# Optimization experiments

Hardware: AMD Instinct MI355X
Metric: run time of the kernel (lower is better)

Reference implementation:

```python
import jax, jax.numpy as jnp
import numpy as np

B, T, D, H = 4, 2048, 1024, 16
DH = D // H


def setup_inputs() -> dict:
    key = jax.random.key(0)
    ks = jax.random.split(key, 5)
    x = jax.random.normal(ks[0], (B, T, D), dtype=jnp.float32)
    W_qkv = jax.random.normal(ks[1], (D, 3 * D), dtype=jnp.float32) * 0.02
    b_qkv = jax.random.normal(ks[2], (3 * D,), dtype=jnp.float32) * 0.02
    W_o = jax.random.normal(ks[3], (D, D), dtype=jnp.float32) * 0.02
    b_o = jax.random.normal(ks[4], (D,), dtype=jnp.float32) * 0.02
    return {"x": x, "W_qkv": W_qkv, "b_qkv": b_qkv, "W_o": W_o, "b_o": b_o}


def reference(x, W_qkv, b_qkv, W_o, b_o):
    b, t, d = x.shape
    qkv = x @ W_qkv + b_qkv                      # [b, t, 3*d]
    # 'b t (k h dh) -> k b h t dh'
    qkv = qkv.reshape(b, t, 3, H, DH).transpose(2, 0, 3, 1, 4)
    q, k, v = qkv[0], qkv[1], qkv[2]             # each [b, h, t, dh]
    scores = jnp.einsum('bhqd,bhkd->bhqk', q, k) / jnp.sqrt(jnp.float32(DH))
    causal_mask = jnp.triu(jnp.ones((t, t), dtype=bool), k=1)  # True above diag
    scores = jnp.where(causal_mask, -jnp.inf, scores)
    attn = jax.nn.softmax(scores, axis=-1)       # [b, h, t, t]
    o = jnp.einsum('bhqk,bhkd->bqhd', attn, v).reshape(b, t, d)
    return o @ W_o + b_o
```

## Files before the change

kernel.cpp:

```cpp
#include <hip/hip_runtime.h>
#include <hip/hip_bf16.h>

typedef __attribute__((ext_vector_type(8))) short bh8;
typedef __attribute__((ext_vector_type(4))) float f32x4;

#define GBL(p) (const __attribute__((address_space(1))) void*)(p)
#define LDSP(p) (__attribute__((address_space(3))) void*)(p)

__device__ __forceinline__ ushort f2bf(float f){
  union { float f; unsigned u; } v; v.f = f;
  unsigned u = v.u;
  return (ushort)((u + 0x7fffu + ((u >> 16) & 1u)) >> 16);
}

__global__ __launch_bounds__(256) void cast_x_kernel(const float4* __restrict__ in,
                                                     ushort* __restrict__ out){
  int i = blockIdx.x * 256 + threadIdx.x;
  float4 v = in[i];
  ushort4 o;
  o.x = f2bf(v.x); o.y = f2bf(v.y); o.z = f2bf(v.z); o.w = f2bf(v.w);
  *(ushort4*)&out[(size_t)i * 4] = o;
}

__global__ __launch_bounds__(256) void transpose_cast_kernel(const float* __restrict__ in,
                                                             ushort* __restrict__ out,
                                                             int R, int C){
  __shared__ float tile[32][33];
  int bx = blockIdx.x * 32;
  int by = blockIdx.y * 32;
  int tx = threadIdx.x, ty = threadIdx.y;
  #pragma unroll
  for (int i = 0; i < 32; i += 8)
    tile[ty + i][tx] = in[(size_t)(by + ty + i) * C + bx + tx];
  __syncthreads();
  #pragma unroll
  for (int i = 0; i < 32; i += 8)
    out[(size_t)(bx + ty + i) * R + by + tx] = f2bf(tile[tx][ty + i]);
}

__global__ __launch_bounds__(256) void gemm_qkv_kernel(
    const ushort* __restrict__ A,
    const ushort* __restrict__ Bt,
    const float* __restrict__ bias,
    ushort* __restrict__ Qd, ushort* __restrict__ Kd, ushort* __restrict__ Vt)
{
  constexpr int K = 1024;
  __shared__ ushort sA[8192];
  __shared__ ushort sB[8192];
  const int tid = threadIdx.x;
  const int lane = tid & 63, wave = tid >> 6;
  const int quad = lane >> 4, l16 = lane & 15;
  const int wm = (wave >> 1) * 64, wn = (wave & 1) * 64;
  const size_t aBase = (size_t)blockIdx.x * 128 * K;
  const size_t bBase = (size_t)blockIdx.y * 128 * K;
  f32x4 acc[4][4] = {};
  for (int k0 = 0; k0 < K; k0 += 64){
    #pragma unroll
    for (int c = 0; c < 4; c++){
      int u = c * 256 + tid;
      int ks = u >> 9, row = (u >> 2) & 127, q = u & 3;
      __builtin_amdgcn_global_load_lds(GBL(A + aBase + (size_t)row * K + k0 + ks * 32 + q * 8),
                                       LDSP(&sA[u * 8]), 16, 0, 0);
      __builtin_amdgcn_global_load_lds(GBL(Bt + bBase + (size_t)row * K + k0 + ks * 32 + q * 8),
                                       LDSP(&sB[u * 8]), 16, 0, 0);
    }
    __syncthreads();
    #pragma unroll
    for (int ks = 0; ks < 2; ks++){
      bh8 af[4], bf[4];
      #pragma unroll
      for (int i = 0; i < 4; i++) af[i] = *(const bh8*)&sA[ks * 4096 + (wm + i * 16 + l16) * 32 + quad * 8];
      #pragma unroll
      for (int j = 0; j < 4; j++) bf[j] = *(const bh8*)&sB[ks * 4096 + (wn + j * 16 + l16) * 32 + quad * 8];
      #pragma unroll
      for (int i = 0; i < 4; i++)
        #pragma unroll
        for (int j = 0; j < 4; j++)
          acc[i][j] = __builtin_amdgcn_mfma_f32_16x16x32_bf16(af[i], bf[j], acc[i][j], 0, 0, 0);
    }
    __syncthreads();
  }
  const int whichBlk = (blockIdx.y * 128) >> 10;
  #pragma unroll
  for (int i = 0; i < 4; i++){
    int mg = blockIdx.x * 128 + wm + i * 16 + quad * 4;
    int bb = mg >> 11, t0 = mg & 2047;
    #pragma unroll
    for (int j = 0; j < 4; j++){
      int ng = blockIdx.y * 128 + wn + j * 16 + l16;
      float bv = bias[ng];
      int h = (ng >> 6) & 15;
      int dh = ng & 63;
      if (whichBlk == 2){
        ushort4 o;
        o.x = f2bf(acc[i][j][0] + bv);
        o.y = f2bf(acc[i][j][1] + bv);
        o.z = f2bf(acc[i][j][2] + bv);
        o.w = f2bf(acc[i][j][3] + bv);
        *(ushort4*)&Vt[((size_t)((bb * 16 + h) * 64 + dh)) * 2048 + t0] = o;
      } else {
        ushort* dst = (whichBlk == 0) ? Qd : Kd;
        float sc = (whichBlk == 0) ? 0.125f : 1.0f;
        #pragma unroll
        for (int r = 0; r < 4; r++)
          dst[((size_t)((bb * 16 + h) * 2048 + t0 + r) << 6) + dh] = f2bf((acc[i][j][r] + bv) * sc);
      }
    }
  }
}

__global__ __launch_bounds__(256, 2) void flash_attn_kernel(
    const ushort* __restrict__ Qd, const ushort* __restrict__ Kd,
    const ushort* __restrict__ Vt, ushort* __restrict__ Od)
{
  __shared__ ushort sK[2][4096];
  __shared__ ushort sV[2][4096];
  __shared__ ushort sP[4][2][1024];
  const int tid = threadIdx.x;
  const int lane = tid & 63, wave = tid >> 6;
  const int quad = lane >> 4, l16 = lane & 15;
  const int bh = blockIdx.x, pairI = blockIdx.y;
  const size_t base = (size_t)bh * (2048 * 64);
  const float M = 5.0f;

  const int p0 = tid, p1 = 256 + tid;
  const int r0 = p0 >> 3, c0 = (p0 & 7) ^ (r0 & 7);
  const int r1 = p1 >> 3, c1 = (p1 & 7) ^ (r1 & 7);
  const ushort* kp0 = Kd + base + r0 * 64 + c0 * 8;
  const ushort* kp1 = Kd + base + r1 * 64 + c1 * 8;
  const ushort* vp0 = Vt + base + (size_t)r0 * 2048 + c0 * 8;
  const ushort* vp1 = Vt + base + (size_t)r1 * 2048 + c1 * 8;

  const int b = bh >> 4, h = bh & 15;

  #pragma unroll 1
  for (int phase = 0; phase < 2; phase++){
    const int qt = phase ? pairI : (15 - pairI);
    const int ktmax = 2 * qt + 1;
    bh8 qf[2][2];
    #pragma unroll
    for (int s = 0; s < 2; s++){
      const ushort* qrow = Qd + base + (size_t)(qt * 128 + s * 64 + wave * 16 + l16) * 64 + quad * 8;
      qf[s][0] = *(const bh8*)qrow;
      qf[s][1] = *(const bh8*)(qrow + 32);
    }
    f32x4 Oacc[2][4] = {};
    float lpart[2][4] = {{0.f,0.f,0.f,0.f},{0.f,0.f,0.f,0.f}};

    __syncthreads();
    __builtin_amdgcn_global_load_lds(GBL(kp0), LDSP(&sK[0][p0 * 8]), 16, 0, 0);
    __builtin_amdgcn_global_load_lds(GBL(kp1), LDSP(&sK[0][p1 * 8]), 16, 0, 0);
    __builtin_amdgcn_global_load_lds(GBL(vp0), LDSP(&sV[0][p0 * 8]), 16, 0, 0);
    __builtin_amdgcn_global_load_lds(GBL(vp1), LDSP(&sV[0][p1 * 8]), 16, 0, 0);

    #pragma unroll 1
    for (int kt = 0; kt <= ktmax; kt++){
      const int buf = kt & 1;
      __syncthreads();
      if (kt < ktmax){
        const int nb = buf ^ 1;
        __builtin_amdgcn_global_load_lds(GBL(kp0 + (kt + 1) * 4096), LDSP(&sK[nb][p0 * 8]), 16, 0, 0);
        __builtin_amdgcn_global_load_lds(GBL(kp1 + (kt + 1) * 4096), LDSP(&sK[nb][p1 * 8]), 16, 0, 0);
        __builtin_amdgcn_global_load_lds(GBL(vp0 + (kt + 1) * 64),   LDSP(&sV[nb][p0 * 8]), 16, 0, 0);
        __builtin_amdgcn_global_load_lds(GBL(vp1 + (kt + 1) * 64),   LDSP(&sV[nb][p1 * 8]), 16, 0, 0);
      }
      const bool act0 = (kt < ktmax);
      f32x4 S[2][4] = {};
      #pragma unroll
      for (int ks = 0; ks < 2; ks++){
        #pragma unroll
        for (int j = 0; j < 4; j++){
          int row = j * 16 + l16;
          int u = row * 8 + ((ks * 4 + quad) ^ (row & 7));
          bh8 bk = *(const bh8*)&sK[buf][u * 8];
          if (act0) S[0][j] = __builtin_amdgcn_mfma_f32_16x16x32_bf16(qf[0][ks], bk, S[0][j], 0, 0, 0);
          S[1][j] = __builtin_amdgcn_mfma_f32_16x16x32_bf16(qf[1][ks], bk, S[1][j], 0, 0, 0);
        }
      }
      if (kt >= ktmax - 1){
        const int sd = (kt == ktmax) ? 1 : 0;
        #pragma unroll
        for (int j = 0; j < 4; j++)
          #pragma unroll
          for (int r = 0; r < 4; r++){
            int relq = wave * 16 + quad * 4 + r;
            int relt = j * 16 + l16;
            if (relt > relq) S[sd][j][r] = -1e30f;
          }
      }
      #pragma unroll
      for (int s = 0; s < 2; s++){
        if (s == 0 && !act0) continue;
        #pragma unroll
        for (int j = 0; j < 4; j++){
          float pv[4];
          #pragma unroll
          for (int r = 0; r < 4; r++){
            pv[r] = __expf(S[s][j][r] - M);
            lpart[s][r] += pv[r];
          }
          __hip_bfloat162 pk0 = __float22bfloat162_rn({pv[0], pv[1]});
          __hip_bfloat162 pk1 = __float22bfloat162_rn({pv[2], pv[3]});
          ushort2 w0 = *(ushort2*)&pk0, w1 = *(ushort2*)&pk1;
          ushort w[4] = {w0.x, w0.y, w1.x, w1.y};
          #pragma unroll
          for (int r = 0; r < 4; r++){
            int row = quad * 4 + r;
            int cu = 2 * j + (l16 >> 3);
            int phys = row * 8 + (cu ^ (row & 7));
            sP[wave][s][phys * 8 + (l16 & 7)] = w[r];
          }
        }
      }
      #pragma unroll
      for (int ks = 0; ks < 2; ks++){
        int up = l16 * 8 + ((ks * 4 + quad) ^ (l16 & 7));
        bh8 ap0, ap1;
        if (act0) ap0 = *(const bh8*)&sP[wave][0][up * 8];
        ap1 = *(const bh8*)&sP[wave][1][up * 8];
        #pragma unroll
        for (int j = 0; j < 4; j++){
          int row = j * 16 + l16;
          int u = row * 8 + ((ks * 4 + quad) ^ (row & 7));
          bh8 bv = *(const bh8*)&sV[buf][u * 8];
          if (act0) Oacc[0][j] = __builtin_amdgcn_mfma_f32_16x16x32_bf16(ap0, bv, Oacc[0][j], 0, 0, 0);
          Oacc[1][j] = __builtin_amdgcn_mfma_f32_16x16x32_bf16(ap1, bv, Oacc[1][j], 0, 0, 0);
        }
      }
    }
    #pragma unroll
    for (int s = 0; s < 2; s++){
      float lr[4];
      #pragma unroll
      for (int r = 0; r < 4; r++){
        float sm = lpart[s][r];
        sm += __shfl_xor(sm, 1, 64);
        sm += __shfl_xor(sm, 2, 64);
        sm += __shfl_xor(sm, 4, 64);
        sm += __shfl_xor(sm, 8, 64);
        lr[r] = 1.0f / sm;
      }
      #pragma unroll
      for (int j = 0; j < 4; j++)
        #pragma unroll
        for (int r = 0; r < 4; r++){
          int qg = qt * 128 + s * 64 + wave * 16 + quad * 4 + r;
          int dh = j * 16 + l16;
          Od[(size_t)(b * 2048 + qg) * 1024 + h * 64 + dh] = f2bf(Oacc[s][j][r] * lr[r]);
        }
    }
  }
}

__global__ __launch_bounds__(256) void gemm_out_kernel(
    const ushort* __restrict__ A,
    const ushort* __restrict__ Bt,
    const float* __restrict__ bias,
    float* __restrict__ out)
{
  constexpr int K = 1024;
  __shared__ ushort smem[12288];
  ushort* sA = smem;
  ushort* sB = smem + 8192;
  const int tid = threadIdx.x;
  const int lane = tid & 63, wave = tid >> 6;
  const int quad = lane >> 4, l16 = lane & 15;
  const int wm = (wave >> 1) * 64, wn = (wave & 1) * 32;
  const size_t aBase = (size_t)blockIdx.x * 128 * K;
  const size_t bBase = (size_t)blockIdx.y * 64 * K;
  f32x4 acc[4][2] = {};
  for (int k0 = 0; k0 < K; k0 += 64){
    #pragma unroll
    for (int c = 0; c < 4; c++){
      int u = c * 256 + tid;
      int ks = u >> 9, row = (u >> 2) & 127, q = u & 3;
      __builtin_amdgcn_global_load_lds(GBL(A + aBase + (size_t)row * K + k0 + ks * 32 + q * 8),
                                       LDSP(&sA[u * 8]), 16, 0, 0);
    }
    #pragma unroll
    for (int c = 0; c < 2; c++){
      int u = c * 256 + tid;
      int ks = u >> 8, row = (u >> 2) & 63, q = u & 3;
      __builtin_amdgcn_global_load_lds(GBL(Bt + bBase + (size_t)row * K + k0 + ks * 32 + q * 8),
                                       LDSP(&sB[u * 8]), 16, 0, 0);
    }
    __syncthreads();
    #pragma unroll
    for (int ks = 0; ks < 2; ks++){
      bh8 af[4], bf[2];
      #pragma unroll
      for (int i = 0; i < 4; i++) af[i] = *(const bh8*)&sA[ks * 4096 + (wm + i * 16 + l16) * 32 + quad * 8];
      #pragma unroll
      for (int j = 0; j < 2; j++) bf[j] = *(const bh8*)&sB[ks * 2048 + (wn + j * 16 + l16) * 32 + quad * 8];
      #pragma unroll
      for (int i = 0; i < 4; i++)
        #pragma unroll
        for (int j = 0; j < 2; j++)
          acc[i][j] = __builtin_amdgcn_mfma_f32_16x16x32_bf16(af[i], bf[j], acc[i][j], 0, 0, 0);
    }
    __syncthreads();
  }
  #pragma unroll
  for (int i = 0; i < 4; i++){
    int gm = blockIdx.x * 128 + wm + i * 16 + quad * 4;
    #pragma unroll
    for (int j = 0; j < 2; j++){
      int ng = blockIdx.y * 64 + wn + j * 16 + l16;
      float bv = bias[ng];
      #pragma unroll
      for (int r = 0; r < 4; r++)
        out[(size_t)(gm + r) * 1024 + ng] = acc[i][j][r] + bv;
    }
  }
}

extern "C" void kernel_launch(void* const* d_in, const int* in_sizes, int n_in,
                              void* d_out, int out_size, void* d_ws, size_t ws_size,
                              hipStream_t stream) {
  const float* x    = (const float*)d_in[0];
  const float* Wqkv = (const float*)d_in[1];
  const float* bqkv = (const float*)d_in[2];
  const float* Wo   = (const float*)d_in[3];
  const float* bo   = (const float*)d_in[4];
  float* out = (float*)d_out;

  char* p = (char*)d_ws;
  ushort* xb  = (ushort*)p;
  ushort* WqT = (ushort*)(p + 16777216);
  ushort* WoT = (ushort*)(p + 16777216 + 6291456);
  ushort* Qd  = (ushort*)(p + 25165824);
  ushort* Kd  = (ushort*)(p + 25165824 + 16777216);
  ushort* Vt  = (ushort*)(p + 25165824 + 33554432);
  ushort* Od  = xb;

  cast_x_kernel<<<8192, 256, 0, stream>>>((const float4*)x, xb);
  transpose_cast_kernel<<<dim3(96, 32), dim3(32, 8), 0, stream>>>(Wqkv, WqT, 1024, 3072);
  transpose_cast_kernel<<<dim3(32, 32), dim3(32, 8), 0, stream>>>(Wo, WoT, 1024, 1024);
  gemm_qkv_kernel<<<dim3(64, 24), 256, 0, stream>>>(xb, WqT, bqkv, Qd, Kd, Vt);
  flash_attn_kernel<<<dim3(64, 8), 256, 0, stream>>>(Qd, Kd, Vt, Od);
  gemm_out_kernel<<<dim3(64, 16), 256, 0, stream>>>(Od, WoT, bo, out);
}
```

Measured before the change: 268.7 us.

## Process paired query tiles jointly in attention and split-K the output GEMM

The flash attention kernel now handles its low and high query tiles in a single key-tile sweep rather than two sequential phases. This shares K/V loads and LDS fragment reads across both tiles and cuts the number of passes and barriers. The output projection GEMM moves to 128x128 tiles with a two-way split over K, writing one partial to a scratch buffer that a separate combine kernel adds back. The cost is higher register pressure in attention, an extra fp32 partial buffer round trip, and an additional launch.

```diff
diff --git a/kernel.cpp b/kernel.cpp
--- a/kernel.cpp
+++ b/kernel.cpp
@@ -115,13 +115,15 @@
 {
   __shared__ ushort sK[2][4096];
   __shared__ ushort sV[2][4096];
-  __shared__ ushort sP[4][2][1024];
+  __shared__ ushort sP[4][4][1024];
   const int tid = threadIdx.x;
   const int lane = tid & 63, wave = tid >> 6;
   const int quad = lane >> 4, l16 = lane & 15;
-  const int bh = blockIdx.x, pairI = blockIdx.y;
+  const int bh = blockIdx.x, p = blockIdx.y;
   const size_t base = (size_t)bh * (2048 * 64);
   const float M = 5.0f;
+  const int qtL = p, qtH = 15 - p;
+  const int ktend = 2 * qtH + 1;
 
   const int p0 = tid, p1 = 256 + tid;
   const int r0 = p0 >> 3, c0 = (p0 & 7) ^ (r0 & 7);
@@ -133,52 +135,61 @@
 
   const int b = bh >> 4, h = bh & 15;
 
-  #pragma unroll 1
-  for (int phase = 0; phase < 2; phase++){
-    const int qt = phase ? pairI : (15 - pairI);
-    const int ktmax = 2 * qt + 1;
-    bh8 qf[2][2];
+  bh8 qf[2][2][2];
+  #pragma unroll
+  for (int t = 0; t < 2; t++){
+    int qt = t ? qtH : qtL;
     #pragma unroll
     for (int s = 0; s < 2; s++){
       const ushort* qrow = Qd + base + (size_t)(qt * 128 + s * 64 + wave * 16 + l16) * 64 + quad * 8;
-      qf[s][0] = *(const bh8*)qrow;
-      qf[s][1] = *(const bh8*)(qrow + 32);
-    }
-    f32x4 Oacc[2][4] = {};
-    float lpart[2][4] = {{0.f,0.f,0.f,0.f},{0.f,0.f,0.f,0.f}};
-
-    __syncthreads();
-    __builtin_amdgcn_global_load_lds(GBL(kp0), LDSP(&sK[0][p0 * 8]), 16, 0, 0);
-    __builtin_amdgcn_global_load_lds(GBL(kp1), LDSP(&sK[0][p1 * 8]), 16, 0, 0);
-    __builtin_amdgcn_global_load_lds(GBL(vp0), LDSP(&sV[0][p0 * 8]), 16, 0, 0);
-    __builtin_amdgcn_global_load_lds(GBL(vp1), LDSP(&sV[0][p1 * 8]), 16, 0, 0);
-
-    #pragma unroll 1
-    for (int kt = 0; kt <= ktmax; kt++){
-      const int buf = kt & 1;
-      __syncthreads();
-      if (kt < ktmax){
-        const int nb = buf ^ 1;
-        __builtin_amdgcn_global_load_lds(GBL(kp0 + (kt + 1) * 4096), LDSP(&sK[nb][p0 * 8]), 16, 0, 0);
-        __builtin_amdgcn_global_load_lds(GBL(kp1 + (kt + 1) * 4096), LDSP(&sK[nb][p1 * 8]), 16, 0, 0);
-        __builtin_amdgcn_global_load_lds(GBL(vp0 + (kt + 1) * 64),   LDSP(&sV[nb][p0 * 8]), 16, 0, 0);
-        __builtin_amdgcn_global_load_lds(GBL(vp1 + (kt + 1) * 64),   LDSP(&sV[nb][p1 * 8]), 16, 0, 0);
-      }
-      const bool act0 = (kt < ktmax);
+      qf[t][s][0] = *(const bh8*)qrow;
+      qf[t][s][1] = *(const bh8*)(qrow + 32);
+    }
+  }
+  f32x4 Oacc[2][2][4] = {};
+  float lpart[2][2][4] = {};
+
+  __builtin_amdgcn_global_load_lds(GBL(kp0), LDSP(&sK[0][p0 * 8]), 16, 0, 0);
+  __builtin_amdgcn_global_load_lds(GBL(kp1), LDSP(&sK[0][p1 * 8]), 16, 0, 0);
+  __builtin_amdgcn_global_load_lds(GBL(vp0), LDSP(&sV[0][p0 * 8]), 16, 0, 0);
+  __builtin_amdgcn_global_load_lds(GBL(vp1), LDSP(&sV[0][p1 * 8]), 16, 0, 0);
+
+  #pragma unroll 1
+  for (int kt = 0; kt <= ktend; kt++){
+    const int buf = kt & 1;
+    __syncthreads();
+    if (kt < ktend){
+      const int nb = buf ^ 1;
+      __builtin_amdgcn_global_load_lds(GBL(kp0 + (kt + 1) * 4096), LDSP(&sK[nb][p0 * 8]), 16, 0, 0);
+      __builtin_amdgcn_global_load_lds(GBL(kp1 + (kt + 1) * 4096), LDSP(&sK[nb][p1 * 8]), 16, 0, 0);
+      __builtin_amdgcn_global_load_lds(GBL(vp0 + (kt + 1) * 64),   LDSP(&sV[nb][p0 * 8]), 16, 0, 0);
+      __builtin_amdgcn_global_load_lds(GBL(vp1 + (kt + 1) * 64),   LDSP(&sV[nb][p1 * 8]), 16, 0, 0);
+    }
+    bh8 bk[2][4];
+    #pragma unroll
+    for (int ks = 0; ks < 2; ks++)
+      #pragma unroll
+      for (int j = 0; j < 4; j++){
+        int row = j * 16 + l16;
+        int u = row * 8 + ((ks * 4 + quad) ^ (row & 7));
+        bk[ks][j] = *(const bh8*)&sK[buf][u * 8];
+      }
+    #pragma unroll
+    for (int t = 0; t < 2; t++){
+      const int qt = t ? qtH : qtL;
+      const int lim = 2 * qt + 1;
+      if (kt > lim) continue;
+      const bool full0 = (kt < lim);
       f32x4 S[2][4] = {};
       #pragma unroll
-      for (int ks = 0; ks < 2; ks++){
+      for (int ks = 0; ks < 2; ks++)
         #pragma unroll
         for (int j = 0; j < 4; j++){
-          int row = j * 16 + l16;
-          int u = row * 8 + ((ks * 4 + quad) ^ (row & 7));
-          bh8 bk = *(const bh8*)&sK[buf][u * 8];
-          if (act0) S[0][j] = __builtin_amdgcn_mfma_f32_16x16x32_bf16(qf[0][ks], bk, S[0][j], 0, 0, 0);
-          S[1][j] = __builtin_amdgcn_mfma_f32_16x16x32_bf16(qf[1][ks], bk, S[1][j], 0, 0, 0);
+          if (full0) S[0][j] = __builtin_amdgcn_mfma_f32_16x16x32_bf16(qf[t][0][ks], bk[ks][j], S[0][j], 0, 0, 0);
+          S[1][j] = __builtin_amdgcn_mfma_f32_16x16x32_bf16(qf[t][1][ks], bk[ks][j], S[1][j], 0, 0, 0);
         }
-      }
-      if (kt >= ktmax - 1){
-        const int sd = (kt == ktmax) ? 1 : 0;
+      if (kt >= lim - 1){
+        const int sd = (kt == lim) ? 1 : 0;
         #pragma unroll
         for (int j = 0; j < 4; j++)
           #pragma unroll
@@ -190,14 +201,14 @@
       }
       #pragma unroll
       for (int s = 0; s < 2; s++){
-        if (s == 0 && !act0) continue;
+        if (s == 0 && !full0) continue;
         #pragma unroll
         for (int j = 0; j < 4; j++){
           float pv[4];
           #pragma unroll
           for (int r = 0; r < 4; r++){
             pv[r] = __expf(S[s][j][r] - M);
-            lpart[s][r] += pv[r];
+            lpart[t][s][r] += pv[r];
           }
           __hip_bfloat162 pk0 = __float22bfloat162_rn({pv[0], pv[1]});
           __hip_bfloat162 pk1 = __float22bfloat162_rn({pv[2], pv[3]});
@@ -208,32 +219,49 @@
             int row = quad * 4 + r;
             int cu = 2 * j + (l16 >> 3);
             int phys = row * 8 + (cu ^ (row & 7));
-            sP[wave][s][phys * 8 + (l16 & 7)] = w[r];
+            sP[wave][t * 2 + s][phys * 8 + (l16 & 7)] = w[r];
           }
         }
       }
+    }
+    bh8 bv[2][4];
+    #pragma unroll
+    for (int ks = 0; ks < 2; ks++)
+      #pragma unroll
+      for (int j = 0; j < 4; j++){
+        int row = j * 16 + l16;
+        int u = row * 8 + ((ks * 4 + quad) ^ (row & 7));
+        bv[ks][j] = *(const bh8*)&sV[buf][u * 8];
+      }
+    #pragma unroll
+    for (int t = 0; t < 2; t++){
+      const int qt = t ? qtH : qtL;
+      const int lim = 2 * qt + 1;
+      if (kt > lim) continue;
+      const bool full0 = (kt < lim);
       #pragma unroll
       for (int ks = 0; ks < 2; ks++){
         int up = l16 * 8 + ((ks * 4 + quad) ^ (l16 & 7));
         bh8 ap0, ap1;
-        if (act0) ap0 = *(const bh8*)&sP[wave][0][up * 8];
-        ap1 = *(const bh8*)&sP[wave][1][up * 8];
+        if (full0) ap0 = *(const bh8*)&sP[wave][t * 2 + 0][up * 8];
+        ap1 = *(const bh8*)&sP[wave][t * 2 + 1][up * 8];
         #pragma unroll
         for (int j = 0; j < 4; j++){
-          int row = j * 16 + l16;
-          int u = row * 8 + ((ks * 4 + quad) ^ (row & 7));
-          bh8 bv = *(const bh8*)&sV[buf][u * 8];
-          if (act0) Oacc[0][j] = __builtin_amdgcn_mfma_f32_16x16x32_bf16(ap0, bv, Oacc[0][j], 0, 0, 0);
-          Oacc[1][j] = __builtin_amdgcn_mfma_f32_16x16x32_bf16(ap1, bv, Oacc[1][j], 0, 0, 0);
+          if (full0) Oacc[t][0][j] = __builtin_amdgcn_mfma_f32_16x16x32_bf16(ap0, bv[ks][j], Oacc[t][0][j], 0, 0, 0);
+          Oacc[t][1][j] = __builtin_amdgcn_mfma_f32_16x16x32_bf16(ap1, bv[ks][j], Oacc[t][1][j], 0, 0, 0);
         }
       }
     }
+  }
+  #pragma unroll
+  for (int t = 0; t < 2; t++){
+    const int qt = t ? qtH : qtL;
     #pragma unroll
     for (int s = 0; s < 2; s++){
       float lr[4];
       #pragma unroll
       for (int r = 0; r < 4; r++){
-        float sm = lpart[s][r];
+        float sm = lpart[t][s][r];
         sm += __shfl_xor(sm, 1, 64);
         sm += __shfl_xor(sm, 2, 64);
         sm += __shfl_xor(sm, 4, 64);
@@ -246,7 +274,7 @@
         for (int r = 0; r < 4; r++){
           int qg = qt * 128 + s * 64 + wave * 16 + quad * 4 + r;
           int dh = j * 16 + l16;
-          Od[(size_t)(b * 2048 + qg) * 1024 + h * 64 + dh] = f2bf(Oacc[s][j][r] * lr[r]);
+          Od[(size_t)(b * 2048 + qg) * 1024 + h * 64 + dh] = f2bf(Oacc[t][s][j][r] * lr[r]);
         }
     }
   }
@@ -256,46 +284,42 @@
     const ushort* __restrict__ A,
     const ushort* __restrict__ Bt,
     const float* __restrict__ bias,
-    float* __restrict__ out)
+    float* __restrict__ out,
+    float* __restrict__ pb)
 {
   constexpr int K = 1024;
-  __shared__ ushort smem[12288];
-  ushort* sA = smem;
-  ushort* sB = smem + 8192;
+  __shared__ ushort sA[8192];
+  __shared__ ushort sB[8192];
   const int tid = threadIdx.x;
   const int lane = tid & 63, wave = tid >> 6;
   const int quad = lane >> 4, l16 = lane & 15;
-  const int wm = (wave >> 1) * 64, wn = (wave & 1) * 32;
+  const int wm = (wave >> 1) * 64, wn = (wave & 1) * 64;
+  const int kz = blockIdx.z;
   const size_t aBase = (size_t)blockIdx.x * 128 * K;
-  const size_t bBase = (size_t)blockIdx.y * 64 * K;
-  f32x4 acc[4][2] = {};
-  for (int k0 = 0; k0 < K; k0 += 64){
+  const size_t bBase = (size_t)blockIdx.y * 128 * K;
+  f32x4 acc[4][4] = {};
+  for (int k0 = kz * 512; k0 < kz * 512 + 512; k0 += 64){
     #pragma unroll
     for (int c = 0; c < 4; c++){
       int u = c * 256 + tid;
       int ks = u >> 9, row = (u >> 2) & 127, q = u & 3;
       __builtin_amdgcn_global_load_lds(GBL(A + aBase + (size_t)row * K + k0 + ks * 32 + q * 8),
                                        LDSP(&sA[u * 8]), 16, 0, 0);
-    }
-    #pragma unroll
-    for (int c = 0; c < 2; c++){
-      int u = c * 256 + tid;
-      int ks = u >> 8, row = (u >> 2) & 63, q = u & 3;
       __builtin_amdgcn_global_load_lds(GBL(Bt + bBase + (size_t)row * K + k0 + ks * 32 + q * 8),
                                        LDSP(&sB[u * 8]), 16, 0, 0);
     }
     __syncthreads();
     #pragma unroll
     for (int ks = 0; ks < 2; ks++){
-      bh8 af[4], bf[2];
+      bh8 af[4], bf[4];
       #pragma unroll
       for (int i = 0; i < 4; i++) af[i] = *(const bh8*)&sA[ks * 4096 + (wm + i * 16 + l16) * 32 + quad * 8];
       #pragma unroll
-      for (int j = 0; j < 2; j++) bf[j] = *(const bh8*)&sB[ks * 2048 + (wn + j * 16 + l16) * 32 + quad * 8];
+      for (int j = 0; j < 4; j++) bf[j] = *(const bh8*)&sB[ks * 4096 + (wn + j * 16 + l16) * 32 + quad * 8];
       #pragma unroll
       for (int i = 0; i < 4; i++)
         #pragma unroll
-        for (int j = 0; j < 2; j++)
+        for (int j = 0; j < 4; j++)
           acc[i][j] = __builtin_amdgcn_mfma_f32_16x16x32_bf16(af[i], bf[j], acc[i][j], 0, 0, 0);
     }
     __syncthreads();
@@ -304,14 +328,28 @@
   for (int i = 0; i < 4; i++){
     int gm = blockIdx.x * 128 + wm + i * 16 + quad * 4;
     #pragma unroll
-    for (int j = 0; j < 2; j++){
-      int ng = blockIdx.y * 64 + wn + j * 16 + l16;
-      float bv = bias[ng];
-      #pragma unroll
-      for (int r = 0; r < 4; r++)
-        out[(size_t)(gm + r) * 1024 + ng] = acc[i][j][r] + bv;
-    }
-  }
+    for (int j = 0; j < 4; j++){
+      int ng = blockIdx.y * 128 + wn + j * 16 + l16;
+      if (kz == 0){
+        float bv = bias[ng];
+        #pragma unroll
+        for (int r = 0; r < 4; r++)
+          out[(size_t)(gm + r) * 1024 + ng] = acc[i][j][r] + bv;
+      } else {
+        #pragma unroll
+        for (int r = 0; r < 4; r++)
+          pb[(size_t)(gm + r) * 1024 + ng] = acc[i][j][r];
+      }
+    }
+  }
+}
+
+__global__ __launch_bounds__(256) void combine_kernel(float4* __restrict__ out,
+                                                      const float4* __restrict__ pb){
+  int i = blockIdx.x * 256 + threadIdx.x;
+  float4 a = out[i], c = pb[i];
+  a.x += c.x; a.y += c.y; a.z += c.z; a.w += c.w;
+  out[i] = a;
 }
 
 extern "C" void kernel_launch(void* const* d_in, const int* in_sizes, int n_in,
@@ -332,11 +370,13 @@
   ushort* Kd  = (ushort*)(p + 25165824 + 16777216);
   ushort* Vt  = (ushort*)(p + 25165824 + 33554432);
   ushort* Od  = xb;
+  float*  pb  = (float*)(p + 25165824);
 
   cast_x_kernel<<<8192, 256, 0, stream>>>((const float4*)x, xb);
   transpose_cast_kernel<<<dim3(96, 32), dim3(32, 8), 0, stream>>>(Wqkv, WqT, 1024, 3072);
   transpose_cast_kernel<<<dim3(32, 32), dim3(32, 8), 0, stream>>>(Wo, WoT, 1024, 1024);
   gemm_qkv_kernel<<<dim3(64, 24), 256, 0, stream>>>(xb, WqT, bqkv, Qd, Kd, Vt);
   flash_attn_kernel<<<dim3(64, 8), 256, 0, stream>>>(Qd, Kd, Vt, Od);
-  gemm_out_kernel<<<dim3(64, 16), 256, 0, stream>>>(Od, WoT, bo, out);
-}
+  gemm_out_kernel<<<dim3(64, 8, 2), 256, 0, stream>>>(Od, WoT, bo, out, pb);
+  combine_kernel<<<8192, 256, 0, stream>>>((float4*)out, (const float4*)pb);
+}
```

Measured after the change: 283.8 us. 1.06x slower.
